# Kernel tuning notes

Measured on AMD Instinct MI355X. Metric: run time of the kernel, lower is better.

## Reference

```python
import jax, jax.numpy as jnp
import numpy as np

N_NODES = 50000
N_RAND_EDGES = 800000
D = 128


def setup_inputs() -> dict:
    key = jax.random.key(0)
    ks = jax.random.split(key, 16)
    # random edges + self loops (docstring: self loops added to avoid zero in-degree)
    src_r = jax.random.randint(ks[0], (N_RAND_EDGES,), 0, N_NODES, dtype=jnp.int32)
    dst_r = jax.random.randint(ks[1], (N_RAND_EDGES,), 0, N_NODES, dtype=jnp.int32)
    loop = jnp.arange(N_NODES, dtype=jnp.int32)
    src = jnp.concatenate([src_r, loop])
    dst = jnp.concatenate([dst_r, loop])
    E = src.shape[0]
    edge_weight = jax.random.uniform(ks[2], (E,), dtype=jnp.float32, minval=0.05, maxval=1.0)
    feats = jax.random.normal(ks[3], (N_NODES, D), dtype=jnp.float32)
    s = 1.0 / np.sqrt(D)
    params = {}
    for i in range(3):
        params[f'W_self{i}'] = jax.random.normal(ks[4 + 3 * i], (D, D), dtype=jnp.float32) * s
        params[f'W_neigh{i}'] = jax.random.normal(ks[5 + 3 * i], (D, D), dtype=jnp.float32) * s
        params[f'b{i}'] = jnp.zeros((D,), dtype=jnp.float32)
    return dict(feats=feats, edge_weight=edge_weight,
                W_self0=params['W_self0'], W_neigh0=params['W_neigh0'], b0=params['b0'],
                W_self1=params['W_self1'], W_neigh1=params['W_neigh1'], b1=params['b1'],
                W_self2=params['W_self2'], W_neigh2=params['W_neigh2'], b2=params['b2'],
                src=src, dst=dst)


def reference(feats, edge_weight, W_self0, W_neigh0, b0, W_self1, W_neigh1, b1,
              W_self2, W_neigh2, b2, src, dst):
    N = feats.shape[0]
    seg = lambda x, ids: jax.ops.segment_sum(x, ids, num_segments=N)
    # EdgeWeightNorm('both'): w_ij / sqrt(out_deg_w(src) * in_deg_w(dst))
    deg_dst = seg(edge_weight, dst)  # weighted in-degree [N]
    deg_src = seg(edge_weight, src)  # weighted out-degree [N]
    denom = jnp.sqrt(jnp.maximum(deg_src[src] * deg_dst[dst], 1e-12))
    w = edge_weight / denom  # [E]
    # unweighted in-degree for DGL fn.mean
    in_deg = jnp.maximum(seg(jnp.ones_like(edge_weight), dst), 1.0)  # [N]

    def sage_layer(h, Ws, Wn, b, act):
        # GraphNorm(None) is identity. SAGEConv mean aggregator with edge weights:
        # m_e = w_e * h[src_e]; neigh_v = mean over in-edges of v
        msgs = w[:, None] * h[src]            # [E, D] (memory-bound gather)
        neigh = seg(msgs, dst) / in_deg[:, None]  # [N, D]
        out = h @ Ws + neigh @ Wn + b
        return jax.nn.relu(out) if act else out

    h = sage_layer(feats, W_self0, W_neigh0, b0, True)
    h = sage_layer(h, W_self1, W_neigh1, b1, True)
    h = sage_layer(h, W_self2, W_neigh2, b2, False)
    return h
```

## Files before the change

### kernel.cpp

```cpp
#include <hip/hip_runtime.h>
#include <hip/hip_bf16.h>

#define D 128
#define BS 256
#define CHUNK 4096
#define CAP 8192

typedef __attribute__((ext_vector_type(8))) short short8v;
typedef __attribute__((ext_vector_type(4))) float f32x4;

__device__ __forceinline__ ushort f2bf(float f) {
    uint u = __float_as_uint(f);
    return (ushort)((u + 0x7fffu + ((u >> 16) & 1u)) >> 16);
}
__device__ __forceinline__ float bf2f(ushort s) {
    return __uint_as_float(((uint)s) << 16);
}


__global__ void cvt_all(const float* __restrict__ feats,
                        const float* __restrict__ Ws0, const float* __restrict__ Wn0,
                        const float* __restrict__ Ws1, const float* __restrict__ Wn1,
                        const float* __restrict__ Ws2, const float* __restrict__ Wn2,
                        ushort* __restrict__ hb, ushort* __restrict__ Wt,
                        int* __restrict__ cursD, int* __restrict__ cursS,
                        int n8, int FB) {
    int tid = threadIdx.x;
    if (blockIdx.x == 0) {
        cursD[tid] = tid * CAP;
        cursS[tid] = tid * CAP;
    }
    if (blockIdx.x < FB) {
        int i = blockIdx.x * 256 + tid;
        if (i >= n8) return;
        const float4* f4 = (const float4*)feats + (size_t)i * 2;
        float4 a = f4[0], b = f4[1];
        uint4 o;
        o.x = (uint)f2bf(a.x) | ((uint)f2bf(a.y) << 16);
        o.y = (uint)f2bf(a.z) | ((uint)f2bf(a.w) << 16);
        o.z = (uint)f2bf(b.x) | ((uint)f2bf(b.y) << 16);
        o.w = (uint)f2bf(b.z) | ((uint)f2bf(b.w) << 16);
        *((uint4*)hb + i) = o;
        return;
    }
    int wb = blockIdx.x - FB;
    int layer = wb >> 7;
    int n = wb & 127;
    int k = tid;
    const float* Ws = (layer == 0) ? Ws0 : (layer == 1) ? Ws1 : Ws2;
    const float* Wn = (layer == 0) ? Wn0 : (layer == 1) ? Wn1 : Wn2;
    float v = (k < 128) ? Ws[k * D + n] : Wn[(k - 128) * D + n];
    Wt[(size_t)layer * 32768 + n * 256 + k] = f2bf(v);
}


__global__ void partition_kernel(const int* __restrict__ src, const int* __restrict__ dst,
                                 const float* __restrict__ ew,
                                 int* __restrict__ cursD, int* __restrict__ cursS,
                                 int2* __restrict__ bufD, int2* __restrict__ bufS, int E) {
    __shared__ int hD[256], hS[256];
    __shared__ int bD[256], bS[256];
    int tid = threadIdx.x, blk = blockIdx.x;
    hD[tid] = 0; hS[tid] = 0;
    __syncthreads();
    int e0 = blk * CHUNK;
    int e1 = e0 + CHUNK < E ? e0 + CHUNK : E;
    for (int e = e0 + tid; e < e1; e += BS) {
        atomicAdd(&hD[dst[e] >> 8], 1);
        atomicAdd(&hS[src[e] >> 8], 1);
    }
    __syncthreads();
    int cD = hD[tid], cS = hS[tid];
    if (cD > 0) bD[tid] = atomicAdd(&cursD[tid], cD);
    if (cS > 0) bS[tid] = atomicAdd(&cursS[tid], cS);
    __syncthreads();
    for (int e = e0 + tid; e < e1; e += BS) {
        int s = src[e], d = dst[e];
        int w = __float_as_int(ew[e]);
        int pD = atomicAdd(&bD[d >> 8], 1);
        bufD[pD] = make_int2(((d & 255) << 16) | s, w);
        int pS = atomicAdd(&bS[s >> 8], 1);
        bufS[pS] = make_int2(s, w);
    }
}


__global__ void srcdeg_kernel(const int2* __restrict__ bufS, const int* __restrict__ cursS,
                              float* __restrict__ rs, int N) {
    __shared__ float acc[256];
    int tid = threadIdx.x, b = blockIdx.x;
    acc[tid] = 0.f;
    __syncthreads();
    int base = b * CAP;
    int end = cursS[b];
    for (int i = base + tid; i < end; i += BS) {
        int2 v = bufS[i];
        atomicAdd(&acc[v.x & 255], __int_as_float(v.y));
    }
    __syncthreads();
    int node = (b << 8) + tid;
    if (node < N) rs[node] = rsqrtf(acc[tid]);
}


__global__ void csr_kernel(const int2* __restrict__ bufD, const int* __restrict__ cursD,
                           const float* __restrict__ rs, int2* __restrict__ begend,
                           int2* __restrict__ csrb, int N) {
    __shared__ int lcnt[256];
    __shared__ float lw[256];
    __shared__ int sc[256];
    int tid = threadIdx.x, b = blockIdx.x;
    lcnt[tid] = 0; lw[tid] = 0.f;
    __syncthreads();
    int base = b * CAP;
    int end = cursD[b];
    for (int i = base + tid; i < end; i += BS) {
        int2 v = bufD[i];
        int l = v.x >> 16;
        atomicAdd(&lcnt[l], 1);
        atomicAdd(&lw[l], __int_as_float(v.y));
    }
    __syncthreads();
    int myc = lcnt[tid];
    float myw = lw[tid];
    sc[tid] = myc;
    __syncthreads();
    for (int off = 1; off < 256; off <<= 1) {
        int t = (tid >= off) ? sc[tid - off] : 0;
        __syncthreads();
        sc[tid] += t;
        __syncthreads();
    }
    int lbase = base + sc[tid] - myc;
    int node = (b << 8) + tid;
    if (node < N) begend[node] = make_int2(lbase, base + sc[tid]);
    lcnt[tid] = lbase;
    lw[tid] = (myc > 0) ? rsqrtf(myw) / (float)myc : 0.f;
    __syncthreads();
    for (int i = base + tid; i < end; i += BS) {
        int2 v = bufD[i];
        int l = v.x >> 16;
        int s = v.x & 0xFFFF;
        float w = __int_as_float(v.y) * rs[s] * lw[l];
        int p = atomicAdd(&lcnt[l], 1);
        csrb[p] = make_int2(s, __float_as_int(w));
    }
}


__global__ void aggregate_bf(const ushort* __restrict__ h, const int2* __restrict__ begend,
                             const int2* __restrict__ csr, ushort* __restrict__ nbuf, int N) {
    int node = (blockIdx.x * blockDim.x + threadIdx.x) >> 6;
    int lane = threadIdx.x & 63;
    if (node >= N) return;
    int2 be = begend[node];
    const uint* hs = (const uint*)h;
    float ax[8], ay[8];
    #pragma unroll
    for (int j = 0; j < 8; ++j) { ax[j] = 0.f; ay[j] = 0.f; }
    int i = be.x;
    for (; i + 8 <= be.y; i += 8) {
        int2 e[8];
        #pragma unroll
        for (int j = 0; j < 8; ++j) e[j] = csr[i + j];
        uint x[8];
        #pragma unroll
        for (int j = 0; j < 8; ++j) x[j] = hs[(size_t)e[j].x * 64 + lane];
        #pragma unroll
        for (int j = 0; j < 8; ++j) {
            float w = __int_as_float(e[j].y);
            ax[j] += w * bf2f((ushort)x[j]);
            ay[j] += w * bf2f((ushort)(x[j] >> 16));
        }
    }
    for (; i < be.y; ++i) {
        int2 e0 = csr[i];
        float w = __int_as_float(e0.y);
        uint x0 = hs[(size_t)e0.x * 64 + lane];
        ax[0] += w * bf2f((ushort)x0);
        ay[0] += w * bf2f((ushort)(x0 >> 16));
    }
    float sx = ((ax[0] + ax[1]) + (ax[2] + ax[3])) + ((ax[4] + ax[5]) + (ax[6] + ax[7]));
    float sy = ((ay[0] + ay[1]) + (ay[2] + ay[3])) + ((ay[4] + ay[5]) + (ay[6] + ay[7]));
    uint o = (uint)f2bf(sx) | ((uint)f2bf(sy) << 16);
    ((uint*)nbuf)[(size_t)node * 64 + lane] = o;
}


#define AST2 40

__global__ __launch_bounds__(256, 4) void mfma_gemm(
    const ushort* __restrict__ A1, const ushort* __restrict__ A2,
    const ushort* __restrict__ Wt, const float* __restrict__ bias,
    ushort* __restrict__ outb, float* __restrict__ outf, int N, int relu) {
    __shared__ ushort As[2][64][AST2];
    __shared__ ushort Bs[2][128][AST2];

    int tid = threadIdx.x;
    int lane = tid & 63;
    int w = tid >> 6;
    int m0 = (w >> 1) * 32, n0 = (w & 1) * 64;
    int row0 = blockIdx.x * 64;
    int q = lane >> 4, li = lane & 15;

    int r1 = tid >> 2, c = tid & 3;
    int gr1 = min(row0 + r1, N - 1);

    uint4 sa0, sb0, sb1;

    sa0 = *(const uint4*)(A1 + (size_t)gr1 * D + c * 8);
    sb0 = *(const uint4*)(Wt + (size_t)r1 * 256 + c * 8);
    sb1 = *(const uint4*)(Wt + (size_t)(r1 + 64) * 256 + c * 8);
    *(uint4*)&As[0][r1][c * 8] = sa0;
    *(uint4*)&Bs[0][r1][c * 8] = sb0;
    *(uint4*)&Bs[0][r1 + 64][c * 8] = sb1;
    __syncthreads();

    f32x4 zero = {0.f, 0.f, 0.f, 0.f};
    f32x4 acc[2][4];
    #pragma unroll
    for (int mf = 0; mf < 2; ++mf)
        #pragma unroll
        for (int nf = 0; nf < 4; ++nf) acc[mf][nf] = zero;

    for (int kc = 0; kc < 8; ++kc) {
        int b = kc & 1;
        if (kc < 7) {
            int nc = kc + 1;
            const ushort* Ak = ((nc < 4) ? A1 : A2) + (nc & 3) * 32;
            sa0 = *(const uint4*)(Ak + (size_t)gr1 * D + c * 8);
            const ushort* Wk = Wt + nc * 32;
            sb0 = *(const uint4*)(Wk + (size_t)r1 * 256 + c * 8);
            sb1 = *(const uint4*)(Wk + (size_t)(r1 + 64) * 256 + c * 8);
        }

        union FragU { uint2 u[2]; short8v v; };
        FragU fa[2], fb[4];
        #pragma unroll
        for (int mf = 0; mf < 2; ++mf) {
            const ushort* p = &As[b][m0 + mf * 16 + li][0];
            fa[mf].u[0] = *(const uint2*)(p + 4 * q);
            fa[mf].u[1] = *(const uint2*)(p + 16 + 4 * q);
        }
        #pragma unroll
        for (int nf = 0; nf < 4; ++nf) {
            const ushort* p = &Bs[b][n0 + nf * 16 + li][0];
            fb[nf].u[0] = *(const uint2*)(p + 4 * q);
            fb[nf].u[1] = *(const uint2*)(p + 16 + 4 * q);
        }
        #pragma unroll
        for (int mf = 0; mf < 2; ++mf)
            #pragma unroll
            for (int nf = 0; nf < 4; ++nf)
                acc[mf][nf] = __builtin_amdgcn_mfma_f32_16x16x32_bf16(
                    fa[mf].v, fb[nf].v, acc[mf][nf], 0, 0, 0);

        if (kc < 7) {
            int b2 = b ^ 1;
            *(uint4*)&As[b2][r1][c * 8] = sa0;
            *(uint4*)&Bs[b2][r1][c * 8] = sb0;
            *(uint4*)&Bs[b2][r1 + 64][c * 8] = sb1;
        }
        __syncthreads();
    }

    #pragma unroll
    for (int nf = 0; nf < 4; ++nf) {
        int n = n0 + nf * 16 + li;
        float bn = bias[n];
        #pragma unroll
        for (int mf = 0; mf < 2; ++mf) {
            #pragma unroll
            for (int p = 0; p < 4; ++p) {
                int gr = row0 + m0 + mf * 16 + q * 4 + p;
                if (gr >= N) continue;
                float v = acc[mf][nf][p] + bn;
                if (relu) v = fmaxf(v, 0.f);
                if (outf) outf[(size_t)gr * D + n] = v;
                else outb[(size_t)gr * D + n] = f2bf(v);
            }
        }
    }
}


extern "C" void kernel_launch(void* const* d_in, const int* in_sizes, int n_in,
                              void* d_out, int out_size, void* d_ws, size_t ws_size,
                              hipStream_t stream) {
    const float* feats = (const float*)d_in[0];
    const float* ew    = (const float*)d_in[1];
    const float* Wself[3]  = {(const float*)d_in[2], (const float*)d_in[5], (const float*)d_in[8]};
    const float* Wneigh[3] = {(const float*)d_in[3], (const float*)d_in[6], (const float*)d_in[9]};
    const float* bias[3]   = {(const float*)d_in[4], (const float*)d_in[7], (const float*)d_in[10]};
    const int* src = (const int*)d_in[11];
    const int* dst = (const int*)d_in[12];

    int N = in_sizes[0] / D;
    int E = in_sizes[11];
    int NB = (N + 255) >> 8;
    int EB = (E + CHUNK - 1) / CHUNK;

    char* ws = (char*)d_ws;
    size_t p = 0;
    auto align256 = [&]() { p = (p + 255) & ~(size_t)255; };

    int* cursD = (int*)(ws + p); p += 256 * 4;             align256();
    int* cursS = (int*)(ws + p); p += 256 * 4;             align256();
    int2* bufD = (int2*)(ws + p); p += (size_t)NB * CAP * 8; align256();
    int2* bufS = (int2*)(ws + p); p += (size_t)NB * CAP * 8; align256();
    int2* csrb = (int2*)(ws + p); p += (size_t)NB * CAP * 8; align256();
    int2* begend = (int2*)(ws + p); p += (size_t)N * 8;    align256();
    float* rs  = (float*)(ws + p); p += (size_t)N * 4;     align256();
    ushort* hA = (ushort*)(ws + p); p += (size_t)N * D * 2; align256();
    ushort* hB = (ushort*)(ws + p); p += (size_t)N * D * 2; align256();
    ushort* nbuf = (ushort*)(ws + p); p += (size_t)N * D * 2; align256();
    ushort* Wt = (ushort*)(ws + p); p += (size_t)3 * 128 * 256 * 2; align256();
    (void)ws_size; (void)n_in; (void)out_size;

    int n8 = N * D / 8;
    int FB = (n8 + 255) / 256;
    cvt_all<<<FB + 384, 256, 0, stream>>>(feats, Wself[0], Wneigh[0], Wself[1], Wneigh[1],
                                          Wself[2], Wneigh[2], hA, Wt, cursD, cursS, n8, FB);
    partition_kernel<<<EB, BS, 0, stream>>>(src, dst, ew, cursD, cursS, bufD, bufS, E);
    srcdeg_kernel<<<NB, BS, 0, stream>>>(bufS, cursS, rs, N);
    csr_kernel<<<NB, BS, 0, stream>>>(bufD, cursD, rs, begend, csrb, N);

    int gb = (N + 63) / 64;
    ushort* hin = hA;
    ushort* houts[3] = {hB, hA, nullptr};
    for (int Lr = 0; Lr < 3; ++Lr) {
        aggregate_bf<<<(N + 3) / 4, 256, 0, stream>>>(hin, begend, csrb, nbuf, N);
        mfma_gemm<<<gb, 256, 0, stream>>>(hin, nbuf, Wt + (size_t)Lr * 32768, bias[Lr],
                                          houts[Lr], (Lr == 2) ? (float*)d_out : nullptr,
                                          N, (Lr < 2) ? 1 : 0);
        hin = houts[Lr];
    }
}
```

Baseline: 241.2 us.

## Fuse neighbor aggregation into the MFMA GEMM via LDS-resident neighbor tile

Merges the separate aggregation and GEMM kernels into one 512-thread kernel per layer. Each block first gathers and aggregates neighbor features for its 64 rows into shared memory, then runs the bf16 MFMA GEMM, taking the neighbor half of K from LDS instead of a global nbuf. This removes the nbuf write/read round trip and one launch per layer. In exchange, the gather phase has less parallelism per block (each wave handles 8 nodes sequentially) and more LDS per block, which may reduce occupancy and latency hiding for the memory-bound gather.

Result: slower. 303.8 us (+26.0%).

```diff
diff --git a/kernel.cpp b/kernel.cpp
--- a/kernel.cpp
+++ b/kernel.cpp
@@ -148,102 +148,111 @@
 }
 
 
-__global__ void aggregate_bf(const ushort* __restrict__ h, const int2* __restrict__ begend,
-                             const int2* __restrict__ csr, ushort* __restrict__ nbuf, int N) {
-    int node = (blockIdx.x * blockDim.x + threadIdx.x) >> 6;
-    int lane = threadIdx.x & 63;
-    if (node >= N) return;
-    int2 be = begend[node];
-    const uint* hs = (const uint*)h;
-    float ax[8], ay[8];
-    #pragma unroll
-    for (int j = 0; j < 8; ++j) { ax[j] = 0.f; ay[j] = 0.f; }
-    int i = be.x;
-    for (; i + 8 <= be.y; i += 8) {
-        int2 e[8];
-        #pragma unroll
-        for (int j = 0; j < 8; ++j) e[j] = csr[i + j];
-        uint x[8];
-        #pragma unroll
-        for (int j = 0; j < 8; ++j) x[j] = hs[(size_t)e[j].x * 64 + lane];
-        #pragma unroll
-        for (int j = 0; j < 8; ++j) {
-            float w = __int_as_float(e[j].y);
-            ax[j] += w * bf2f((ushort)x[j]);
-            ay[j] += w * bf2f((ushort)(x[j] >> 16));
-        }
-    }
-    for (; i < be.y; ++i) {
-        int2 e0 = csr[i];
-        float w = __int_as_float(e0.y);
-        uint x0 = hs[(size_t)e0.x * 64 + lane];
-        ax[0] += w * bf2f((ushort)x0);
-        ay[0] += w * bf2f((ushort)(x0 >> 16));
-    }
-    float sx = ((ax[0] + ax[1]) + (ax[2] + ax[3])) + ((ax[4] + ax[5]) + (ax[6] + ax[7]));
-    float sy = ((ay[0] + ay[1]) + (ay[2] + ay[3])) + ((ay[4] + ay[5]) + (ay[6] + ay[7]));
-    uint o = (uint)f2bf(sx) | ((uint)f2bf(sy) << 16);
-    ((uint*)nbuf)[(size_t)node * 64 + lane] = o;
-}
-
-
 #define AST2 40
-
-__global__ __launch_bounds__(256, 4) void mfma_gemm(
-    const ushort* __restrict__ A1, const ushort* __restrict__ A2,
-    const ushort* __restrict__ Wt, const float* __restrict__ bias,
-    ushort* __restrict__ outb, float* __restrict__ outf, int N, int relu) {
+#define NST 132
+
+__global__ __launch_bounds__(512, 4) void fused_layer(
+    const ushort* __restrict__ hin, const int2* __restrict__ begend,
+    const int2* __restrict__ csr, const ushort* __restrict__ Wt,
+    const float* __restrict__ bias, ushort* __restrict__ outb,
+    float* __restrict__ outf, int N, int relu) {
     __shared__ ushort As[2][64][AST2];
     __shared__ ushort Bs[2][128][AST2];
+    __shared__ ushort nLDS[64][NST];
 
     int tid = threadIdx.x;
     int lane = tid & 63;
     int w = tid >> 6;
-    int m0 = (w >> 1) * 32, n0 = (w & 1) * 64;
     int row0 = blockIdx.x * 64;
     int q = lane >> 4, li = lane & 15;
 
+    {
+        const uint* hs = (const uint*)hin;
+        for (int nn = 0; nn < 8; ++nn) {
+            int r = w * 8 + nn;
+            int node = row0 + r;
+            int2 be = (node < N) ? begend[node] : make_int2(0, 0);
+            float ax[8], ay[8];
+            #pragma unroll
+            for (int j = 0; j < 8; ++j) { ax[j] = 0.f; ay[j] = 0.f; }
+            int i = be.x;
+            for (; i + 8 <= be.y; i += 8) {
+                int2 e[8];
+                #pragma unroll
+                for (int j = 0; j < 8; ++j) e[j] = csr[i + j];
+                uint x[8];
+                #pragma unroll
+                for (int j = 0; j < 8; ++j) x[j] = hs[(size_t)e[j].x * 64 + lane];
+                #pragma unroll
+                for (int j = 0; j < 8; ++j) {
+                    float ww = __int_as_float(e[j].y);
+                    ax[j] += ww * bf2f((ushort)x[j]);
+                    ay[j] += ww * bf2f((ushort)(x[j] >> 16));
+                }
+            }
+            for (; i < be.y; ++i) {
+                int2 e0 = csr[i];
+                float ww = __int_as_float(e0.y);
+                uint x0 = hs[(size_t)e0.x * 64 + lane];
+                ax[0] += ww * bf2f((ushort)x0);
+                ay[0] += ww * bf2f((ushort)(x0 >> 16));
+            }
+            float sx = ((ax[0] + ax[1]) + (ax[2] + ax[3])) + ((ax[4] + ax[5]) + (ax[6] + ax[7]));
+            float sy = ((ay[0] + ay[1]) + (ay[2] + ay[3])) + ((ay[4] + ay[5]) + (ay[6] + ay[7]));
+            *(uint*)&nLDS[r][2 * lane] = (uint)f2bf(sx) | ((uint)f2bf(sy) << 16);
+        }
+    }
+    __syncthreads();
+
+    int wr = w >> 2, wc = w & 3;
+    int m0 = wr * 32, n0 = wc * 32;
+
     int r1 = tid >> 2, c = tid & 3;
-    int gr1 = min(row0 + r1, N - 1);
-
-    uint4 sa0, sb0, sb1;
-
-    sa0 = *(const uint4*)(A1 + (size_t)gr1 * D + c * 8);
+    int gra = min(row0 + (tid >> 2), N - 1);
+
+    uint4 sa0, sb0;
+
+    if (tid < 256) sa0 = *(const uint4*)(hin + (size_t)gra * D + c * 8);
     sb0 = *(const uint4*)(Wt + (size_t)r1 * 256 + c * 8);
-    sb1 = *(const uint4*)(Wt + (size_t)(r1 + 64) * 256 + c * 8);
-    *(uint4*)&As[0][r1][c * 8] = sa0;
+    if (tid < 256) *(uint4*)&As[0][tid >> 2][c * 8] = sa0;
     *(uint4*)&Bs[0][r1][c * 8] = sb0;
-    *(uint4*)&Bs[0][r1 + 64][c * 8] = sb1;
     __syncthreads();
 
     f32x4 zero = {0.f, 0.f, 0.f, 0.f};
-    f32x4 acc[2][4];
+    f32x4 acc[2][2];
     #pragma unroll
     for (int mf = 0; mf < 2; ++mf)
         #pragma unroll
-        for (int nf = 0; nf < 4; ++nf) acc[mf][nf] = zero;
+        for (int nf = 0; nf < 2; ++nf) acc[mf][nf] = zero;
 
     for (int kc = 0; kc < 8; ++kc) {
         int b = kc & 1;
         if (kc < 7) {
             int nc = kc + 1;
-            const ushort* Ak = ((nc < 4) ? A1 : A2) + (nc & 3) * 32;
-            sa0 = *(const uint4*)(Ak + (size_t)gr1 * D + c * 8);
-            const ushort* Wk = Wt + nc * 32;
-            sb0 = *(const uint4*)(Wk + (size_t)r1 * 256 + c * 8);
-            sb1 = *(const uint4*)(Wk + (size_t)(r1 + 64) * 256 + c * 8);
+            if (nc < 4 && tid < 256)
+                sa0 = *(const uint4*)(hin + (size_t)gra * D + nc * 32 + c * 8);
+            sb0 = *(const uint4*)(Wt + (size_t)r1 * 256 + nc * 32 + c * 8);
         }
 
         union FragU { uint2 u[2]; short8v v; };
-        FragU fa[2], fb[4];
+        FragU fa[2], fb[2];
+        if (kc < 4) {
+            #pragma unroll
+            for (int mf = 0; mf < 2; ++mf) {
+                const ushort* p = &As[b][m0 + mf * 16 + li][0];
+                fa[mf].u[0] = *(const uint2*)(p + 4 * q);
+                fa[mf].u[1] = *(const uint2*)(p + 16 + 4 * q);
+            }
+        } else {
+            #pragma unroll
+            for (int mf = 0; mf < 2; ++mf) {
+                const ushort* p = &nLDS[m0 + mf * 16 + li][(kc - 4) * 32 + 4 * q];
+                fa[mf].u[0] = *(const uint2*)p;
+                fa[mf].u[1] = *(const uint2*)(p + 16);
+            }
+        }
         #pragma unroll
-        for (int mf = 0; mf < 2; ++mf) {
-            const ushort* p = &As[b][m0 + mf * 16 + li][0];
-            fa[mf].u[0] = *(const uint2*)(p + 4 * q);
-            fa[mf].u[1] = *(const uint2*)(p + 16 + 4 * q);
-        }
-        #pragma unroll
-        for (int nf = 0; nf < 4; ++nf) {
+        for (int nf = 0; nf < 2; ++nf) {
             const ushort* p = &Bs[b][n0 + nf * 16 + li][0];
             fb[nf].u[0] = *(const uint2*)(p + 4 * q);
             fb[nf].u[1] = *(const uint2*)(p + 16 + 4 * q);
@@ -251,21 +260,21 @@
         #pragma unroll
         for (int mf = 0; mf < 2; ++mf)
             #pragma unroll
-            for (int nf = 0; nf < 4; ++nf)
+            for (int nf = 0; nf < 2; ++nf)
                 acc[mf][nf] = __builtin_amdgcn_mfma_f32_16x16x32_bf16(
                     fa[mf].v, fb[nf].v, acc[mf][nf], 0, 0, 0);
 
         if (kc < 7) {
             int b2 = b ^ 1;
-            *(uint4*)&As[b2][r1][c * 8] = sa0;
+            int nc = kc + 1;
+            if (nc < 4 && tid < 256) *(uint4*)&As[b2][tid >> 2][c * 8] = sa0;
             *(uint4*)&Bs[b2][r1][c * 8] = sb0;
-            *(uint4*)&Bs[b2][r1 + 64][c * 8] = sb1;
         }
         __syncthreads();
     }
 
     #pragma unroll
-    for (int nf = 0; nf < 4; ++nf) {
+    for (int nf = 0; nf < 2; ++nf) {
         int n = n0 + nf * 16 + li;
         float bn = bias[n];
         #pragma unroll
@@ -313,7 +322,6 @@
     float* rs  = (float*)(ws + p); p += (size_t)N * 4;     align256();
     ushort* hA = (ushort*)(ws + p); p += (size_t)N * D * 2; align256();
     ushort* hB = (ushort*)(ws + p); p += (size_t)N * D * 2; align256();
-    ushort* nbuf = (ushort*)(ws + p); p += (size_t)N * D * 2; align256();
     ushort* Wt = (ushort*)(ws + p); p += (size_t)3 * 128 * 256 * 2; align256();
     (void)ws_size; (void)n_in; (void)out_size;
 
@@ -329,10 +337,10 @@
     ushort* hin = hA;
     ushort* houts[3] = {hB, hA, nullptr};
     for (int Lr = 0; Lr < 3; ++Lr) {
-        aggregate_bf<<<(N + 3) / 4, 256, 0, stream>>>(hin, begend, csrb, nbuf, N);
-        mfma_gemm<<<gb, 256, 0, stream>>>(hin, nbuf, Wt + (size_t)Lr * 32768, bias[Lr],
-                                          houts[Lr], (Lr == 2) ? (float*)d_out : nullptr,
-                                          N, (Lr < 2) ? 1 : 0);
+        fused_layer<<<gb, 512, 0, stream>>>(hin, begend, csrb, Wt + (size_t)Lr * 32768,
+                                            bias[Lr], houts[Lr],
+                                            (Lr == 2) ? (float*)d_out : nullptr,
+                                            N, (Lr < 2) ? 1 : 0);
         hin = houts[Lr];
     }
 }
```
